# Kernel tuning notes

Measured on AMD Instinct MI355X. Metric: run time of the kernel, lower is better.

## Reference

```python
import jax, jax.numpy as jnp
import numpy as np

B, T, D, H, O = 64, 512, 256, 512, 256


def setup_inputs() -> dict:
    key = jax.random.key(0)
    ks = jax.random.split(key, 9)
    s = 0.05  # weight scale to keep activations in a sane range
    return {
        "x": jax.random.normal(ks[0], (B, T, D), jnp.float32),
        "h0": jax.random.normal(ks[1], (B, H), jnp.float32) * s,
        "c0": jax.random.normal(ks[2], (B, H), jnp.float32) * s,
        "W_x": jax.random.normal(ks[3], (D, 4 * H), jnp.float32) * s,
        "U_h": jax.random.normal(ks[4], (H, 4 * H), jnp.float32) * s,
        "b_ih": jax.random.normal(ks[5], (4 * H,), jnp.float32) * s,
        "b_hh": jax.random.normal(ks[6], (4 * H,), jnp.float32) * s,
        "W_y": jax.random.normal(ks[7], (H, O), jnp.float32) * s,
        "b_y": jax.random.normal(ks[8], (O,), jnp.float32) * s,
    }


def _lstm(x, h0, c0, W_x, U_h, b_ih, b_hh, W_y, b_y):
    Hd = h0.shape[-1]
    # hoist input projection out of the sequential loop: [B,T,4H]
    x_proj = jnp.einsum("btd,dg->btg", x, W_x) + b_ih + b_hh

    def step(carry, xp_t):
        h, c = carry
        gates = xp_t + h @ U_h  # [B,4H]
        i, f, j, o = jnp.split(gates, 4, axis=-1)
        i = jax.nn.sigmoid(i)
        f = jax.nn.sigmoid(f)
        j = jnp.tanh(j)
        o = jax.nn.sigmoid(o)
        c = f * c + i * j
        h = o * jnp.tanh(c)
        return (h, c), h

    (h_T, c_T), hs = jax.lax.scan(step, (h0, c0), jnp.swapaxes(x_proj, 0, 1))
    hs = jnp.swapaxes(hs, 0, 1)  # [B,T,H]
    y_hat = jnp.einsum("bth,ho->bto", hs, W_y) + b_y
    return y_hat, h_T, c_T


def reference(x, h0, c0, W_x, U_h, b_ih, b_hh, W_y, b_y):
    return _lstm(x, h0, c0, W_x, U_h, b_ih, b_hh, W_y, b_y)
```

## Files before the change

kernel.cpp:

```cpp
#include <hip/hip_runtime.h>

typedef short short8 __attribute__((ext_vector_type(8)));
typedef float f32x4 __attribute__((ext_vector_type(4)));

#define AS1 __attribute__((address_space(1)))
#define AS3 __attribute__((address_space(3)))

static constexpr size_t XP_OFF = 0;
static constexpr size_t HS_OFF = 134217728;
static constexpr size_t U_OFF  = 167772160;
static constexpr size_t WX_OFF = 169869312;
static constexpr size_t WY_OFF = 170917888;
static constexpr size_t BI_OFF = 171180032;
static constexpr size_t HB_OFF = 171188224;
static constexpr size_t FL_OFF = 171319296;
static constexpr size_t TB_OFF = 171323392;
static constexpr size_t PR_OFF = 171324416;
static constexpr size_t RS_OFF = 171328512;

static __device__ __forceinline__ unsigned short f2bf(float f) {
  unsigned u = __float_as_uint(f);
  unsigned r = (u + 0x7fffu + ((u >> 16) & 1u)) >> 16;
  return (unsigned short)r;
}
static __device__ __forceinline__ float bf2f(unsigned short s) {
  return __uint_as_float(((unsigned)s) << 16);
}
static __device__ __forceinline__ float sigf(float x) { return 1.0f / (1.0f + __expf(-x)); }
static __device__ __forceinline__ float tanhf_(float x) { return 1.0f - 2.0f / (1.0f + __expf(2.0f * x)); }

static __device__ __forceinline__ void gld_lds16(const void* g, void* l) {
  __builtin_amdgcn_global_load_lds((const AS1 unsigned int*)g, (AS3 unsigned int*)l, 16, 0, 0);
}
template<int SLOW>
static __device__ __forceinline__ void gld_lds16_c(const void* g, void* l) {
  if constexpr (SLOW)
    __builtin_amdgcn_global_load_lds((const AS1 unsigned int*)g, (AS3 unsigned int*)l, 16, 0, 17);
  else
    __builtin_amdgcn_global_load_lds((const AS1 unsigned int*)g, (AS3 unsigned int*)l, 16, 0, 1);
}
template<int SLOW>
static __device__ __forceinline__ unsigned ldflag(const unsigned* p) {
  unsigned r;
  if constexpr (SLOW)
    r = __hip_atomic_load(p, __ATOMIC_RELAXED, __HIP_MEMORY_SCOPE_AGENT);
  else
    asm volatile("global_load_dword %0, %1, off sc0\n\ts_waitcnt vmcnt(0)"
                 : "=v"(r) : "v"(p) : "memory");
  return r;
}
template<int SLOW>
static __device__ __forceinline__ void stflag(unsigned* p, unsigned v) {
  if constexpr (SLOW)
    __hip_atomic_store(p, v, __ATOMIC_RELAXED, __HIP_MEMORY_SCOPE_AGENT);
  else
    asm volatile("global_store_dword %0, %1, off sc0" :: "v"(p), "v"(v) : "memory");
}
template<int SLOW>
static __device__ __forceinline__ void sth32(void* p, unsigned v) {
  if constexpr (SLOW)
    __hip_atomic_store((unsigned*)p, v, __ATOMIC_RELAXED, __HIP_MEMORY_SCOPE_AGENT);
  else
    asm volatile("global_store_dword %0, %1, off sc0" :: "v"(p), "v"(v) : "memory");
}

#define DO16(M) M(0) M(1) M(2) M(3) M(4) M(5) M(6) M(7) M(8) M(9) M(10) M(11) \
  M(12) M(13) M(14) M(15)

static __device__ __forceinline__ unsigned orig_col(unsigned p) {
  return ((p & 127u) >> 5) * 512u + (p >> 7) * 32u + (p & 31u);
}

__global__ void prep_kernel(const float* __restrict__ Wx, const float* __restrict__ Uh,
                            const float* __restrict__ bih, const float* __restrict__ bhh,
                            const float* __restrict__ Wy, const float* __restrict__ h0,
                            char* __restrict__ ws) {
  unsigned idx0 = blockIdx.x * blockDim.x + threadIdx.x;
  unsigned stride = gridDim.x * blockDim.x;
  unsigned short* Up = (unsigned short*)(ws + U_OFF);
  for (unsigned i = idx0; i < 1048576u; i += stride) {
    unsigned k = i & 511u, p = i >> 9;
    Up[i] = f2bf(Uh[k * 2048u + orig_col(p)]);
  }
  unsigned short* Wxp = (unsigned short*)(ws + WX_OFF);
  for (unsigned i = idx0; i < 524288u; i += stride) {
    unsigned k = i & 255u, p = i >> 8;
    Wxp[i] = f2bf(Wx[k * 2048u + orig_col(p)]);
  }
  unsigned short* Wyp = (unsigned short*)(ws + WY_OFF);
  for (unsigned i = idx0; i < 131072u; i += stride) {
    unsigned k = i & 511u, n = i >> 9;
    Wyp[i] = f2bf(Wy[k * 256u + n]);
  }
  float* bp = (float*)(ws + BI_OFF);
  for (unsigned p = idx0; p < 2048u; p += stride) {
    unsigned c = orig_col(p);
    bp[p] = bih[c] + bhh[c];
  }
  unsigned short* hb = (unsigned short*)(ws + HB_OFF);
  for (unsigned i = idx0; i < 32768u; i += stride) hb[i] = f2bf(h0[i]);
  for (unsigned i = idx0; i < 3328u; i += stride)
    ((unsigned*)(ws + FL_OFF))[i] = 0u;
}

__launch_bounds__(256, 1)
__global__ void xproj_kernel(const float* __restrict__ x, char* __restrict__ ws) {
  extern __shared__ char smem[];
  char* a_lds = smem;
  char* b_lds = smem + 65536;
  const int tid = threadIdx.x, lane = tid & 63, wid = tid >> 6;
  const int wm = wid >> 1, wn = wid & 1;
  const int r0 = blockIdx.x * 128, p0 = blockIdx.y * 128;
  const unsigned short* WxT = (const unsigned short*)(ws + WX_OFF);

#pragma unroll
  for (int i = 0; i < 16; ++i) {
    int base = i * 4096 + wid * 1024;
    int byte = base + lane * 16;
    int row = byte >> 9;
    int kb = (byte >> 4) & 31;
    gld_lds16(WxT + (size_t)(p0 + row) * 256 + (size_t)((kb ^ (row & 15)) * 8), b_lds + base);
  }
  {
    int row = tid >> 1, half = tid & 1;
    const float* xr = x + (size_t)(r0 + row) * 256 + half * 128;
    char* ar = a_lds + row * 512;
#pragma unroll
    for (int i = 0; i < 16; ++i) {
      float4 f0 = *(const float4*)(xr + i * 8);
      float4 f1 = *(const float4*)(xr + i * 8 + 4);
      short8 v;
      v[0] = (short)f2bf(f0.x); v[1] = (short)f2bf(f0.y); v[2] = (short)f2bf(f0.z); v[3] = (short)f2bf(f0.w);
      v[4] = (short)f2bf(f1.x); v[5] = (short)f2bf(f1.y); v[6] = (short)f2bf(f1.z); v[7] = (short)f2bf(f1.w);
      int kb = half * 16 + i;
      *(short8*)(ar + ((kb ^ (row & 15)) * 16)) = v;
    }
  }
  __syncthreads();

  typedef float f32x16 __attribute__((ext_vector_type(16)));
  f32x16 acc[2][2] = {};
#pragma unroll
  for (int kk = 0; kk < 16; ++kk) {
    int kbW = kk * 2 + (lane >> 5);
    short8 a[2], b[2];
#pragma unroll
    for (int mt = 0; mt < 2; ++mt) {
      int row = wm * 64 + mt * 32 + (lane & 31);
      a[mt] = *(const short8*)(a_lds + row * 512 + ((kbW ^ (row & 15)) * 16));
    }
#pragma unroll
    for (int nt = 0; nt < 2; ++nt) {
      int n = wn * 64 + nt * 32 + (lane & 31);
      b[nt] = *(const short8*)(b_lds + n * 512 + ((kbW ^ (n & 15)) * 16));
    }
#pragma unroll
    for (int mt = 0; mt < 2; ++mt)
#pragma unroll
      for (int nt = 0; nt < 2; ++nt)
        acc[mt][nt] = __builtin_amdgcn_mfma_f32_32x32x16_bf16(a[mt], b[nt], acc[mt][nt], 0, 0, 0);
  }

  const float* bias = (const float*)(ws + BI_OFF);
  unsigned short* xp = (unsigned short*)(ws + XP_OFF);
#pragma unroll
  for (int nt = 0; nt < 2; ++nt) {
    int p = p0 + wn * 64 + nt * 32 + (lane & 31);
    float bv = bias[p];
    int g = p >> 7, q = p & 127;
#pragma unroll
    for (int mt = 0; mt < 2; ++mt) {
#pragma unroll
      for (int rg = 0; rg < 16; ++rg) {
        int r = r0 + wm * 64 + mt * 32 + (rg & 3) + 8 * (rg >> 2) + 4 * (lane >> 5);
        int b = r >> 9, t = r & 511;
        xp[((size_t)(t * 16 + g) * 64 + b) * 128 + q] = f2bf(acc[mt][nt][rg] + bv);
      }
    }
  }
}

template<int SLOW>
static __device__ __forceinline__ void run_loop(char* smem, const float* c0, char* ws,
                                                float* out, int tid, int ring, int g) {
  char* h_lds = smem;
  float* gates = (float*)(smem + 16384);
  const int lane = tid & 63, wid = tid >> 6;
  const int bq16 = ring * 16;
  char* hbuf = ws + HB_OFF;
  const unsigned short* xp = (const unsigned short*)(ws + XP_OFF);
  unsigned short* hs = (unsigned short*)(ws + HS_OFF);
  unsigned* flags = (unsigned*)(ws + FL_OFF);
  unsigned* myflag = flags + (size_t)(ring * 16 + g) * 16;
  unsigned* pollp = flags + (size_t)(ring * 16 + (lane & 15)) * 16;

  short8 bU[32];
  {
    const unsigned short* Up = (const unsigned short*)(ws + U_OFF);
    const unsigned short* pu0 = Up + (size_t)(g * 128 + wid * 32 + (lane & 15)) * 512 + (lane >> 4) * 8;
    const unsigned short* pu1 = pu0 + 16 * 512;
#define LDU0(k) asm volatile("global_load_dwordx4 %0, %1, off offset:%c2" \
                             : "=v"(bU[k]) : "v"(pu0), "i"((k) * 64) : "memory");
#define LDU1(k) asm volatile("global_load_dwordx4 %0, %1, off offset:%c2" \
                             : "=v"(bU[16 + (k)]) : "v"(pu1), "i"((k) * 64) : "memory");
    DO16(LDU0)
    DO16(LDU1)
#undef LDU0
#undef LDU1
    asm volatile("s_waitcnt vmcnt(0)" ::: "memory");
    __builtin_amdgcn_sched_barrier(0);
  }
  const int bl = tid >> 4, jlp = (tid & 15) * 2;
  float2 cp = *(const float2*)(c0 + (size_t)(bq16 + bl) * 512 + g * 32 + jlp);
  float cc0 = cp.x, cc1 = cp.y;

  for (int t = 0; t < 512; ++t) {
    const unsigned short* xpt = xp + ((size_t)(t * 16 + g) * 64 + (bq16 + bl)) * 128;
    ushort2 xi2 = *(const ushort2*)(xpt + jlp);
    ushort2 xf2 = *(const ushort2*)(xpt + 32 + jlp);
    ushort2 xj2 = *(const ushort2*)(xpt + 64 + jlp);
    ushort2 xo2 = *(const ushort2*)(xpt + 96 + jlp);

    if (wid == 0) {
      unsigned tgt = (unsigned)t;
      while (__any(ldflag<SLOW>(pollp) < tgt)) {}
    }
    __syncthreads();

    const char* hb = hbuf + (t & 1) * 65536;
#pragma unroll
    for (int i = 0; i < 4; ++i) {
      int r = wid * 4 + i;
      gld_lds16_c<SLOW>(hb + (size_t)(bq16 + r) * 1024 + ((lane ^ r) * 16), h_lds + r * 1024);
    }
    __syncthreads();

    f32x4 ac[2][2] = {};
#pragma unroll
    for (int ks = 0; ks < 16; ++ks) {
      int row = lane & 15;
      int gi = (ks * 4 + (lane >> 4)) ^ row;
      short8 a = *(const short8*)(h_lds + row * 1024 + gi * 16);
      ac[0][ks & 1] = __builtin_amdgcn_mfma_f32_16x16x32_bf16(a, bU[ks], ac[0][ks & 1], 0, 0, 0);
      ac[1][ks & 1] = __builtin_amdgcn_mfma_f32_16x16x32_bf16(a, bU[16 + ks], ac[1][ks & 1], 0, 0, 0);
    }
#pragma unroll
    for (int nt = 0; nt < 2; ++nt) {
      f32x4 acc = ac[nt][0] + ac[nt][1];
      int pl = wid * 32 + nt * 16 + (lane & 15);
      int rb = (lane >> 4) * 4;
#pragma unroll
      for (int rg = 0; rg < 4; ++rg)
        gates[(rb + rg) * 132 + pl] = acc[rg];
    }
    __syncthreads();

    const float* gr = gates + bl * 132;
    float2 gi2 = *(const float2*)(gr + jlp);
    float2 gf2 = *(const float2*)(gr + 32 + jlp);
    float2 gj2 = *(const float2*)(gr + 64 + jlp);
    float2 go2 = *(const float2*)(gr + 96 + jlp);
    float i0 = sigf(gi2.x + bf2f(xi2.x)), i1 = sigf(gi2.y + bf2f(xi2.y));
    float f0 = sigf(gf2.x + bf2f(xf2.x)), f1 = sigf(gf2.y + bf2f(xf2.y));
    float j0v = tanhf_(gj2.x + bf2f(xj2.x)), j1v = tanhf_(gj2.y + bf2f(xj2.y));
    float o0 = sigf(go2.x + bf2f(xo2.x)), o1 = sigf(go2.y + bf2f(xo2.y));
    cc0 = f0 * cc0 + i0 * j0v;
    cc1 = f1 * cc1 + i1 * j1v;
    float h0v = o0 * tanhf_(cc0);
    float h1v = o1 * tanhf_(cc1);
    unsigned hv = (unsigned)f2bf(h0v) | ((unsigned)f2bf(h1v) << 16);

    if (t < 511)
      sth32<SLOW>(hbuf + ((t + 1) & 1) * 65536 +
                  ((size_t)(bq16 + bl) * 512 + g * 32 + jlp) * 2, hv);
    *(unsigned*)(hs + ((size_t)(bq16 + bl) * 512 + t) * 512 + g * 32 + jlp) = hv;
    if (t == 511) {
      *(float2*)(out + 8388608u + (size_t)(bq16 + bl) * 512 + g * 32 + jlp) = make_float2(h0v, h1v);
      *(float2*)(out + 8421376u + (size_t)(bq16 + bl) * 512 + g * 32 + jlp) = make_float2(cc0, cc1);
    }
    asm volatile("s_waitcnt vmcnt(0)" ::: "memory");
    __syncthreads();
    if (tid == 0) stflag<SLOW>(myflag, (unsigned)(t + 1));
  }
}

__launch_bounds__(256, 1)
__global__ void lstm_rec_kernel(const float* __restrict__ c0, char* __restrict__ ws,
                                float* __restrict__ out) {
  extern __shared__ char smem[];
  unsigned* ldsT = (unsigned*)(smem + 16384 + 8448);
  unsigned* ldsF = (unsigned*)(smem + 16384 + 8448 + 1024);
  const int tid = threadIdx.x, lane = tid & 63, wid = tid >> 6;
  const int bid = blockIdx.x;

  unsigned* tbl = (unsigned*)(ws + TB_OFF);
  unsigned xcc;
  asm volatile("s_getreg_b32 %0, hwreg(HW_REG_XCC_ID)" : "=s"(xcc));
  if (tid == 0)
    __hip_atomic_store(tbl + bid, (xcc & 15u) + 1u, __ATOMIC_RELAXED, __HIP_MEMORY_SCOPE_AGENT);
  if (wid == 0) {
    for (;;) {
      unsigned v0 = __hip_atomic_load(tbl + lane, __ATOMIC_RELAXED, __HIP_MEMORY_SCOPE_AGENT);
      unsigned v1 = __hip_atomic_load(tbl + 64 + lane, __ATOMIC_RELAXED, __HIP_MEMORY_SCOPE_AGENT);
      unsigned v2 = __hip_atomic_load(tbl + 128 + lane, __ATOMIC_RELAXED, __HIP_MEMORY_SCOPE_AGENT);
      unsigned v3 = __hip_atomic_load(tbl + 192 + lane, __ATOMIC_RELAXED, __HIP_MEMORY_SCOPE_AGENT);
      ldsT[lane] = v0; ldsT[64 + lane] = v1; ldsT[128 + lane] = v2; ldsT[192 + lane] = v3;
      if (__all((v0 != 0u) && (v1 != 0u) && (v2 != 0u) && (v3 != 0u))) break;
    }
  }
  __syncthreads();

  int ringXcd[4] = {0, 0, 0, 0};
  int nr = 0;
  for (int x = 1; x <= 16; ++x) {
    int cnt = 0;
    for (int b = 0; b < 256; ++b) cnt += (ldsT[b] == (unsigned)x) ? 1 : 0;
    if (cnt >= 16 && nr < 4) ringXcd[nr++] = x;
  }
  bool slowForce = (nr < 4);
  int ring = 0, g = 0;
  bool sel = false;
  if (slowForce) {
    sel = (bid < 64);
    ring = bid >> 4;
    g = bid & 15;
  } else {
    unsigned myx = ldsT[bid];
    int r = -1;
    for (int i = 0; i < 4; ++i)
      if (ringXcd[i] == (int)myx) r = i;
    if (r >= 0) {
      int rank = 0;
      for (int b = 0; b < bid; ++b) rank += (ldsT[b] == myx) ? 1 : 0;
      if (rank < 16) { sel = true; ring = r; g = rank; }
    }
  }
  if (!sel) return;

  bool fast = false;
  if (!slowForce) {
    unsigned* probe = (unsigned*)(ws + PR_OFF);
    if (tid == 0) stflag<0>(probe + (size_t)(ring * 16 + g) * 16, 1u);
    asm volatile("s_waitcnt vmcnt(0)" ::: "memory");
    if (wid == 0) {
      int ok = 0;
      for (int it = 0; it < 4096; ++it) {
        unsigned v = ldflag<0>(probe + (size_t)(ring * 16 + (lane & 15)) * 16);
        if (__all(v != 0u)) { ok = 1; break; }
      }
      if (lane == 0) ldsF[0] = (unsigned)ok;
    }
    __syncthreads();
    unsigned ok = ldsF[0];
    unsigned* res = (unsigned*)(ws + RS_OFF);
    if (tid == 0) stflag<1>(res + (size_t)(ring * 16 + g) * 16, ok ? 2u : 1u);
    if (wid == 0) {
      unsigned v;
      do {
        v = ldflag<1>(res + (size_t)(ring * 16 + (lane & 15)) * 16);
      } while (__any(v == 0u));
      if (lane == 0) ldsF[1] = __all(v == 2u) ? 1u : 0u;
    }
    __syncthreads();
    fast = (ldsF[1] != 0u);
  }

  if (fast) run_loop<0>(smem, c0, (char*)ws, out, tid, ring, g);
  else      run_loop<1>(smem, c0, (char*)ws, out, tid, ring, g);
}

__launch_bounds__(256, 1)
__global__ void ygemm_kernel(const char* __restrict__ ws, const float* __restrict__ by,
                             float* __restrict__ out) {
  extern __shared__ char smem[];
  char* a_lds = smem;
  char* b_lds = smem + 32768;
  const int tid = threadIdx.x, lane = tid & 63, wid = tid >> 6;
  const int wm = wid >> 1, wn = wid & 1;
  const int r0 = blockIdx.x * 128, n0 = blockIdx.y * 128;
  const unsigned short* hs = (const unsigned short*)(ws + HS_OFF);
  const unsigned short* WyT = (const unsigned short*)(ws + WY_OFF);

  typedef float f32x16 __attribute__((ext_vector_type(16)));
  f32x16 acc[2][2] = {};
  for (int k0 = 0; k0 < 512; k0 += 128) {
#pragma unroll
    for (int i = 0; i < 8; ++i) {
      int base = i * 4096 + wid * 1024;
      int byte = base + lane * 16;
      int row = byte >> 8;
      int kb = (byte >> 4) & 15;
      gld_lds16(hs + (size_t)(r0 + row) * 512 + k0 + ((kb ^ (row & 15)) * 8), a_lds + base);
      gld_lds16(WyT + (size_t)(n0 + row) * 512 + k0 + ((kb ^ (row & 15)) * 8), b_lds + base);
    }
    __syncthreads();
#pragma unroll
    for (int kk = 0; kk < 8; ++kk) {
      int kbW = kk * 2 + (lane >> 5);
      short8 a[2], b[2];
#pragma unroll
      for (int mt = 0; mt < 2; ++mt) {
        int row = wm * 64 + mt * 32 + (lane & 31);
        a[mt] = *(const short8*)(a_lds + row * 256 + ((kbW ^ (row & 15)) * 16));
        int n = wn * 64 + mt * 32 + (lane & 31);
        b[mt] = *(const short8*)(b_lds + n * 256 + ((kbW ^ (n & 15)) * 16));
      }
#pragma unroll
      for (int mt = 0; mt < 2; ++mt)
#pragma unroll
        for (int nt = 0; nt < 2; ++nt)
          acc[mt][nt] = __builtin_amdgcn_mfma_f32_32x32x16_bf16(a[mt], b[nt], acc[mt][nt], 0, 0, 0);
    }
    __syncthreads();
  }
#pragma unroll
  for (int nt = 0; nt < 2; ++nt) {
    int o = n0 + wn * 64 + nt * 32 + (lane & 31);
    float bv = by[o];
#pragma unroll
    for (int mt = 0; mt < 2; ++mt)
#pragma unroll
      for (int rg = 0; rg < 16; ++rg) {
        int r = r0 + wm * 64 + mt * 32 + (rg & 3) + 8 * (rg >> 2) + 4 * (lane >> 5);
        out[(size_t)r * 256 + o] = acc[mt][nt][rg] + bv;
      }
  }
}

extern "C" void kernel_launch(void* const* d_in, const int* in_sizes, int n_in,
                              void* d_out, int out_size, void* d_ws, size_t ws_size,
                              hipStream_t stream) {
  (void)in_sizes; (void)n_in; (void)out_size; (void)ws_size;
  const float* x   = (const float*)d_in[0];
  const float* h0  = (const float*)d_in[1];
  const float* c0  = (const float*)d_in[2];
  const float* Wx  = (const float*)d_in[3];
  const float* Uh  = (const float*)d_in[4];
  const float* bih = (const float*)d_in[5];
  const float* bhh = (const float*)d_in[6];
  const float* Wy  = (const float*)d_in[7];
  const float* by  = (const float*)d_in[8];
  char* ws = (char*)d_ws;
  float* out = (float*)d_out;

  prep_kernel<<<1024, 256, 0, stream>>>(Wx, Uh, bih, bhh, Wy, h0, ws);
  xproj_kernel<<<dim3(256, 16), 256, 131072, stream>>>(x, ws);
  lstm_rec_kernel<<<256, 256, 16384 + 8448 + 1024 + 64, stream>>>(c0, ws, out);
  ygemm_kernel<<<dim3(256, 2), 256, 65536, stream>>>(ws, by, out);
}
```

Measured before the change: 1.746 ms.

## Use per-wave flags and stream h directly from global into MFMA

Replaces the per-block flag and two block barriers with per-wave progress flags, so each wave publishes its own step completion. Consumers poll all producer wave flags with a ballot mask and load each k-slice of h straight from global memory into registers once its producer chunk is ready. This lets MFMAs start on early chunks while later producers are still finishing, instead of waiting on LDS staging and block syncs. The cost is more flag traffic, four times as many flag slots, and finer-grained polling on the critical path.

```diff
diff --git a/kernel.cpp b/kernel.cpp
--- a/kernel.cpp
+++ b/kernel.cpp
@@ -14,9 +14,9 @@
 static constexpr size_t BI_OFF = 171180032;
 static constexpr size_t HB_OFF = 171188224;
 static constexpr size_t FL_OFF = 171319296;
-static constexpr size_t TB_OFF = 171323392;
-static constexpr size_t PR_OFF = 171324416;
-static constexpr size_t RS_OFF = 171328512;
+static constexpr size_t TB_OFF = 171335680;
+static constexpr size_t PR_OFF = 171336704;
+static constexpr size_t RS_OFF = 171340800;
 
 static __device__ __forceinline__ unsigned short f2bf(float f) {
   unsigned u = __float_as_uint(f);
@@ -33,17 +33,11 @@
   __builtin_amdgcn_global_load_lds((const AS1 unsigned int*)g, (AS3 unsigned int*)l, 16, 0, 0);
 }
 template<int SLOW>
-static __device__ __forceinline__ void gld_lds16_c(const void* g, void* l) {
-  if constexpr (SLOW)
-    __builtin_amdgcn_global_load_lds((const AS1 unsigned int*)g, (AS3 unsigned int*)l, 16, 0, 17);
-  else
-    __builtin_amdgcn_global_load_lds((const AS1 unsigned int*)g, (AS3 unsigned int*)l, 16, 0, 1);
-}
-template<int SLOW>
 static __device__ __forceinline__ unsigned ldflag(const unsigned* p) {
   unsigned r;
   if constexpr (SLOW)
-    r = __hip_atomic_load(p, __ATOMIC_RELAXED, __HIP_MEMORY_SCOPE_AGENT);
+    asm volatile("global_load_dword %0, %1, off sc0 sc1\n\ts_waitcnt vmcnt(0)"
+                 : "=v"(r) : "v"(p) : "memory");
   else
     asm volatile("global_load_dword %0, %1, off sc0\n\ts_waitcnt vmcnt(0)"
                  : "=v"(r) : "v"(p) : "memory");
@@ -99,7 +93,7 @@
   }
   unsigned short* hb = (unsigned short*)(ws + HB_OFF);
   for (unsigned i = idx0; i < 32768u; i += stride) hb[i] = f2bf(h0[i]);
-  for (unsigned i = idx0; i < 3328u; i += stride)
+  for (unsigned i = idx0; i < 6400u; i += stride)
     ((unsigned*)(ws + FL_OFF))[i] = 0u;
 }
 
@@ -183,16 +177,15 @@
 template<int SLOW>
 static __device__ __forceinline__ void run_loop(char* smem, const float* c0, char* ws,
                                                 float* out, int tid, int ring, int g) {
-  char* h_lds = smem;
-  float* gates = (float*)(smem + 16384);
+  float* gates = (float*)smem;
   const int lane = tid & 63, wid = tid >> 6;
   const int bq16 = ring * 16;
   char* hbuf = ws + HB_OFF;
   const unsigned short* xp = (const unsigned short*)(ws + XP_OFF);
   unsigned short* hs = (unsigned short*)(ws + HS_OFF);
   unsigned* flags = (unsigned*)(ws + FL_OFF);
-  unsigned* myflag = flags + (size_t)(ring * 16 + g) * 16;
-  unsigned* pollp = flags + (size_t)(ring * 16 + (lane & 15)) * 16;
+  unsigned* myflag = flags + ((size_t)(ring * 16 + g) * 4 + wid) * 16;
+  const unsigned* pollw = flags + ((size_t)(ring * 16 + (lane >> 2)) * 4 + (lane & 3)) * 16;
 
   short8 bU[32];
   {
@@ -213,6 +206,7 @@
   const int bl = tid >> 4, jlp = (tid & 15) * 2;
   float2 cp = *(const float2*)(c0 + (size_t)(bq16 + bl) * 512 + g * 32 + jlp);
   float cc0 = cp.x, cc1 = cp.y;
+  const char* paB = hbuf + (size_t)(bq16 + (lane & 15)) * 1024 + (lane >> 4) * 16;
 
   for (int t = 0; t < 512; ++t) {
     const unsigned short* xpt = xp + ((size_t)(t * 16 + g) * 64 + (bq16 + bl)) * 128;
@@ -221,37 +215,74 @@
     ushort2 xj2 = *(const ushort2*)(xpt + 64 + jlp);
     ushort2 xo2 = *(const ushort2*)(xpt + 96 + jlp);
 
-    if (wid == 0) {
-      unsigned tgt = (unsigned)t;
-      while (__any(ldflag<SLOW>(pollp) < tgt)) {}
-    }
-    __syncthreads();
-
-    const char* hb = hbuf + (t & 1) * 65536;
-#pragma unroll
-    for (int i = 0; i < 4; ++i) {
-      int r = wid * 4 + i;
-      gld_lds16_c<SLOW>(hb + (size_t)(bq16 + r) * 1024 + ((lane ^ r) * 16), h_lds + r * 1024);
-    }
-    __syncthreads();
-
+    const char* pa = paB + (t & 1) * 65536;
+    const unsigned tgt = (unsigned)t;
+    unsigned long long bm;
+    {
+      unsigned v0 = ldflag<SLOW>(pollw);
+      bm = __ballot(v0 >= tgt);
+    }
     f32x4 ac[2][2] = {};
-#pragma unroll
-    for (int ks = 0; ks < 16; ++ks) {
-      int row = lane & 15;
-      int gi = (ks * 4 + (lane >> 4)) ^ row;
-      short8 a = *(const short8*)(h_lds + row * 1024 + gi * 16);
-      ac[0][ks & 1] = __builtin_amdgcn_mfma_f32_16x16x32_bf16(a, bU[ks], ac[0][ks & 1], 0, 0, 0);
-      ac[1][ks & 1] = __builtin_amdgcn_mfma_f32_16x16x32_bf16(a, bU[16 + ks], ac[1][ks & 1], 0, 0, 0);
-    }
+    short8 F0, F1, F2;
+#define WAITK(ks) while (((bm >> (4 * (ks))) & 15ull) != 15ull) {                \
+      unsigned v_ = ldflag<SLOW>(pollw);                                         \
+      bm = __ballot(v_ >= tgt);                                                  \
+    }
+#define LOADF(R, ks) do {                                                        \
+      if constexpr (SLOW)                                                        \
+        asm volatile("global_load_dwordx4 %0, %1, off offset:%c2 sc0 sc1"        \
+                     : "=v"(R) : "v"(pa), "i"((ks) * 64) : "memory");            \
+      else                                                                       \
+        asm volatile("global_load_dwordx4 %0, %1, off offset:%c2 sc0"            \
+                     : "=v"(R) : "v"(pa), "i"((ks) * 64) : "memory");            \
+    } while (0)
+#define MM2(CUR, ks)                                                             \
+    ac[0][(ks) & 1] = __builtin_amdgcn_mfma_f32_16x16x32_bf16(CUR, bU[(ks)], ac[0][(ks) & 1], 0, 0, 0); \
+    ac[1][(ks) & 1] = __builtin_amdgcn_mfma_f32_16x16x32_bf16(CUR, bU[16 + (ks)], ac[1][(ks) & 1], 0, 0, 0);
+#define STEPK(ks, CUR, NX)                                                       \
+    WAITK((ks) + 2)                                                              \
+    LOADF(NX, (ks) + 2);                                                         \
+    asm volatile("s_waitcnt vmcnt(2)" ::: "memory");                             \
+    __builtin_amdgcn_sched_barrier(0);                                           \
+    MM2(CUR, ks)
+
+    WAITK(0)
+    LOADF(F0, 0);
+    WAITK(1)
+    LOADF(F1, 1);
+    STEPK(0, F0, F2)
+    STEPK(1, F1, F0)
+    STEPK(2, F2, F1)
+    STEPK(3, F0, F2)
+    STEPK(4, F1, F0)
+    STEPK(5, F2, F1)
+    STEPK(6, F0, F2)
+    STEPK(7, F1, F0)
+    STEPK(8, F2, F1)
+    STEPK(9, F0, F2)
+    STEPK(10, F1, F0)
+    STEPK(11, F2, F1)
+    STEPK(12, F0, F2)
+    STEPK(13, F1, F0)
+    asm volatile("s_waitcnt vmcnt(1)" ::: "memory");
+    __builtin_amdgcn_sched_barrier(0);
+    MM2(F2, 14)
+    asm volatile("s_waitcnt vmcnt(0)" ::: "memory");
+    __builtin_amdgcn_sched_barrier(0);
+    MM2(F0, 15)
+#undef STEPK
+#undef MM2
+#undef LOADF
+#undef WAITK
+
 #pragma unroll
     for (int nt = 0; nt < 2; ++nt) {
-      f32x4 acc = ac[nt][0] + ac[nt][1];
+      f32x4 facc = ac[nt][0] + ac[nt][1];
       int pl = wid * 32 + nt * 16 + (lane & 15);
       int rb = (lane >> 4) * 4;
 #pragma unroll
       for (int rg = 0; rg < 4; ++rg)
-        gates[(rb + rg) * 132 + pl] = acc[rg];
+        gates[(rb + rg) * 132 + pl] = facc[rg];
     }
     __syncthreads();
 
@@ -273,14 +304,13 @@
     if (t < 511)
       sth32<SLOW>(hbuf + ((t + 1) & 1) * 65536 +
                   ((size_t)(bq16 + bl) * 512 + g * 32 + jlp) * 2, hv);
+    asm volatile("s_waitcnt vmcnt(0)" ::: "memory");
+    if ((lane & 63) == 0) stflag<SLOW>(myflag, (unsigned)(t + 1));
     *(unsigned*)(hs + ((size_t)(bq16 + bl) * 512 + t) * 512 + g * 32 + jlp) = hv;
     if (t == 511) {
       *(float2*)(out + 8388608u + (size_t)(bq16 + bl) * 512 + g * 32 + jlp) = make_float2(h0v, h1v);
       *(float2*)(out + 8421376u + (size_t)(bq16 + bl) * 512 + g * 32 + jlp) = make_float2(cc0, cc1);
     }
-    asm volatile("s_waitcnt vmcnt(0)" ::: "memory");
-    __syncthreads();
-    if (tid == 0) stflag<SLOW>(myflag, (unsigned)(t + 1));
   }
 }
 
@@ -288,8 +318,8 @@
 __global__ void lstm_rec_kernel(const float* __restrict__ c0, char* __restrict__ ws,
                                 float* __restrict__ out) {
   extern __shared__ char smem[];
-  unsigned* ldsT = (unsigned*)(smem + 16384 + 8448);
-  unsigned* ldsF = (unsigned*)(smem + 16384 + 8448 + 1024);
+  unsigned* ldsT = (unsigned*)smem;
+  unsigned* ldsF = (unsigned*)(smem + 1024);
   const int tid = threadIdx.x, lane = tid & 63, wid = tid >> 6;
   const int bid = blockIdx.x;
 
@@ -357,13 +387,15 @@
     if (wid == 0) {
       unsigned v;
       do {
-        v = ldflag<1>(res + (size_t)(ring * 16 + (lane & 15)) * 16);
+        v = __hip_atomic_load((unsigned*)(ws + RS_OFF) + (size_t)(ring * 16 + (lane & 15)) * 16,
+                              __ATOMIC_RELAXED, __HIP_MEMORY_SCOPE_AGENT);
       } while (__any(v == 0u));
       if (lane == 0) ldsF[1] = __all(v == 2u) ? 1u : 0u;
     }
     __syncthreads();
     fast = (ldsF[1] != 0u);
   }
+  __syncthreads();
 
   if (fast) run_loop<0>(smem, c0, (char*)ws, out, tid, ring, g);
   else      run_loop<1>(smem, c0, (char*)ws, out, tid, ring, g);
@@ -445,6 +477,6 @@
 
   prep_kernel<<<1024, 256, 0, stream>>>(Wx, Uh, bih, bhh, Wy, h0, ws);
   xproj_kernel<<<dim3(256, 16), 256, 131072, stream>>>(x, ws);
-  lstm_rec_kernel<<<256, 256, 16384 + 8448 + 1024 + 64, stream>>>(c0, ws, out);
+  lstm_rec_kernel<<<256, 256, 8448, stream>>>(c0, ws, out);
   ygemm_kernel<<<dim3(256, 2), 256, 65536, stream>>>(ws, by, out);
 }
```

New measurement: 2.567 ms. 47.0% more time.

## Remove per-step block barriers in LSTM recurrence via per-wave flags and in-register gates

Applied to the files above, without the earlier changes.

Reorders the gate columns so that each wave's MFMA output already holds the i,f,j,o values for its own hidden units. Gates are then combined with lane shuffles in registers instead of through an LDS gates buffer guarded by two __syncthreads. Each wave publishes its own progress flag and every wave polls all 64 producer flags, and the h tile in LDS is double-buffered. Together these remove most block-wide barriers from the sequential 512-step loop. The cost is more flag traffic (64 flags polled per wave, larger flag region to clear) and more shuffle work.

```diff
diff --git a/kernel.cpp b/kernel.cpp
--- a/kernel.cpp
+++ b/kernel.cpp
@@ -14,9 +14,9 @@
 static constexpr size_t BI_OFF = 171180032;
 static constexpr size_t HB_OFF = 171188224;
 static constexpr size_t FL_OFF = 171319296;
-static constexpr size_t TB_OFF = 171323392;
-static constexpr size_t PR_OFF = 171324416;
-static constexpr size_t RS_OFF = 171328512;
+static constexpr size_t TB_OFF = 171581440;
+static constexpr size_t PR_OFF = 171582464;
+static constexpr size_t RS_OFF = 171586560;
 
 static __device__ __forceinline__ unsigned short f2bf(float f) {
   unsigned u = __float_as_uint(f);
@@ -43,7 +43,8 @@
 static __device__ __forceinline__ unsigned ldflag(const unsigned* p) {
   unsigned r;
   if constexpr (SLOW)
-    r = __hip_atomic_load(p, __ATOMIC_RELAXED, __HIP_MEMORY_SCOPE_AGENT);
+    asm volatile("global_load_dword %0, %1, off sc0 sc1\n\ts_waitcnt vmcnt(0)"
+                 : "=v"(r) : "v"(p) : "memory");
   else
     asm volatile("global_load_dword %0, %1, off sc0\n\ts_waitcnt vmcnt(0)"
                  : "=v"(r) : "v"(p) : "memory");
@@ -57,18 +58,22 @@
     asm volatile("global_store_dword %0, %1, off sc0" :: "v"(p), "v"(v) : "memory");
 }
 template<int SLOW>
-static __device__ __forceinline__ void sth32(void* p, unsigned v) {
+static __device__ __forceinline__ void sth64(void* p, unsigned long long v) {
   if constexpr (SLOW)
-    __hip_atomic_store((unsigned*)p, v, __ATOMIC_RELAXED, __HIP_MEMORY_SCOPE_AGENT);
+    __hip_atomic_store((unsigned long long*)p, v, __ATOMIC_RELAXED, __HIP_MEMORY_SCOPE_AGENT);
   else
-    asm volatile("global_store_dword %0, %1, off sc0" :: "v"(p), "v"(v) : "memory");
+    asm volatile("global_store_dwordx2 %0, %1, off sc0" :: "v"(p), "v"(v) : "memory");
 }
 
 #define DO16(M) M(0) M(1) M(2) M(3) M(4) M(5) M(6) M(7) M(8) M(9) M(10) M(11) \
   M(12) M(13) M(14) M(15)
 
 static __device__ __forceinline__ unsigned orig_col(unsigned p) {
-  return ((p & 127u) >> 5) * 512u + (p >> 7) * 32u + (p & 31u);
+  unsigned pw = p & 127u, g = p >> 7;
+  unsigned wid = pw >> 5, n = (pw >> 4) & 1u, c = pw & 15u;
+  unsigned gate = n * 2u + (c >> 3);
+  unsigned jl = wid * 8u + (c & 7u);
+  return gate * 512u + g * 32u + jl;
 }
 
 __global__ void prep_kernel(const float* __restrict__ Wx, const float* __restrict__ Uh,
@@ -99,7 +104,7 @@
   }
   unsigned short* hb = (unsigned short*)(ws + HB_OFF);
   for (unsigned i = idx0; i < 32768u; i += stride) hb[i] = f2bf(h0[i]);
-  for (unsigned i = idx0; i < 3328u; i += stride)
+  for (unsigned i = idx0; i < 67840u; i += stride)
     ((unsigned*)(ws + FL_OFF))[i] = 0u;
 }
 
@@ -167,14 +172,18 @@
   for (int nt = 0; nt < 2; ++nt) {
     int p = p0 + wn * 64 + nt * 32 + (lane & 31);
     float bv = bias[p];
-    int g = p >> 7, q = p & 127;
+    int g = p >> 7, pw = p & 127;
+    int widp = pw >> 5, np = (pw >> 4) & 1, cq = pw & 15;
+    int gate = np * 2 + (cq >> 3);
+    int jl = widp * 8 + (cq & 7);
+    int qx = jl * 4 + gate;
 #pragma unroll
     for (int mt = 0; mt < 2; ++mt) {
 #pragma unroll
       for (int rg = 0; rg < 16; ++rg) {
         int r = r0 + wm * 64 + mt * 32 + (rg & 3) + 8 * (rg >> 2) + 4 * (lane >> 5);
         int b = r >> 9, t = r & 511;
-        xp[((size_t)(t * 16 + g) * 64 + b) * 128 + q] = f2bf(acc[mt][nt][rg] + bv);
+        xp[((size_t)(t * 16 + g) * 64 + b) * 128 + qx] = f2bf(acc[mt][nt][rg] + bv);
       }
     }
   }
@@ -183,16 +192,15 @@
 template<int SLOW>
 static __device__ __forceinline__ void run_loop(char* smem, const float* c0, char* ws,
                                                 float* out, int tid, int ring, int g) {
-  char* h_lds = smem;
-  float* gates = (float*)(smem + 16384);
+  char* h_lds2 = smem;
   const int lane = tid & 63, wid = tid >> 6;
   const int bq16 = ring * 16;
   char* hbuf = ws + HB_OFF;
   const unsigned short* xp = (const unsigned short*)(ws + XP_OFF);
   unsigned short* hs = (unsigned short*)(ws + HS_OFF);
   unsigned* flags = (unsigned*)(ws + FL_OFF);
-  unsigned* myflag = flags + (size_t)(ring * 16 + g) * 16;
-  unsigned* pollp = flags + (size_t)(ring * 16 + (lane & 15)) * 16;
+  unsigned* pubp = flags + ((size_t)(ring * 16 + (lane & 15)) * 64 + (g * 4 + wid)) * 16;
+  const unsigned* pollp = flags + ((size_t)(ring * 16 + g) * 64 + lane) * 16;
 
   short8 bU[32];
   {
@@ -210,28 +218,35 @@
     asm volatile("s_waitcnt vmcnt(0)" ::: "memory");
     __builtin_amdgcn_sched_barrier(0);
   }
-  const int bl = tid >> 4, jlp = (tid & 15) * 2;
-  float2 cp = *(const float2*)(c0 + (size_t)(bq16 + bl) * 512 + g * 32 + jlp);
-  float cc0 = cp.x, cc1 = cp.y;
+
+  const int c = lane & 15, rg = lane >> 4;
+  const bool active = (c < 8);
+  const int jl = wid * 8 + (c & 7);
+  const int q = (c >> 2) & 1;
+  const bool odd = (c & 1), hi = ((c >> 1) & 1);
+  float cc[4];
+#pragma unroll
+  for (int r = 0; r < 4; ++r)
+    cc[r] = c0[(size_t)(bq16 + 4 * rg + r) * 512 + g * 32 + jl];
 
   for (int t = 0; t < 512; ++t) {
-    const unsigned short* xpt = xp + ((size_t)(t * 16 + g) * 64 + (bq16 + bl)) * 128;
-    ushort2 xi2 = *(const ushort2*)(xpt + jlp);
-    ushort2 xf2 = *(const ushort2*)(xpt + 32 + jlp);
-    ushort2 xj2 = *(const ushort2*)(xpt + 64 + jlp);
-    ushort2 xo2 = *(const ushort2*)(xpt + 96 + jlp);
-
-    if (wid == 0) {
+    const unsigned short* xpt = xp + ((size_t)(t * 16 + g) * 64 + (bq16 + 4 * rg)) * 128 + jl * 4;
+    ushort4 xg0 = *(const ushort4*)(xpt);
+    ushort4 xg1 = *(const ushort4*)(xpt + 128);
+    ushort4 xg2 = *(const ushort4*)(xpt + 256);
+    ushort4 xg3 = *(const ushort4*)(xpt + 384);
+
+    {
       unsigned tgt = (unsigned)t;
-      while (__any(ldflag<SLOW>(pollp) < tgt)) {}
-    }
-    __syncthreads();
-
+      unsigned v = ldflag<SLOW>(pollp);
+      while (!__all(v >= tgt)) v = ldflag<SLOW>(pollp);
+    }
+    char* hl = h_lds2 + (t & 1) * 16384;
     const char* hb = hbuf + (t & 1) * 65536;
 #pragma unroll
     for (int i = 0; i < 4; ++i) {
       int r = wid * 4 + i;
-      gld_lds16_c<SLOW>(hb + (size_t)(bq16 + r) * 1024 + ((lane ^ r) * 16), h_lds + r * 1024);
+      gld_lds16_c<SLOW>(hb + (size_t)(bq16 + r) * 1024 + ((lane ^ r) * 16), hl + r * 1024);
     }
     __syncthreads();
 
@@ -239,48 +254,66 @@
 #pragma unroll
     for (int ks = 0; ks < 16; ++ks) {
       int row = lane & 15;
-      int gi = (ks * 4 + (lane >> 4)) ^ row;
-      short8 a = *(const short8*)(h_lds + row * 1024 + gi * 16);
+      int gi = (ks * 4 + rg) ^ row;
+      short8 a = *(const short8*)(hl + row * 1024 + gi * 16);
       ac[0][ks & 1] = __builtin_amdgcn_mfma_f32_16x16x32_bf16(a, bU[ks], ac[0][ks & 1], 0, 0, 0);
       ac[1][ks & 1] = __builtin_amdgcn_mfma_f32_16x16x32_bf16(a, bU[16 + ks], ac[1][ks & 1], 0, 0, 0);
     }
-#pragma unroll
-    for (int nt = 0; nt < 2; ++nt) {
-      f32x4 acc = ac[nt][0] + ac[nt][1];
-      int pl = wid * 32 + nt * 16 + (lane & 15);
-      int rb = (lane >> 4) * 4;
-#pragma unroll
-      for (int rg = 0; rg < 4; ++rg)
-        gates[(rb + rg) * 132 + pl] = acc[rg];
-    }
-    __syncthreads();
-
-    const float* gr = gates + bl * 132;
-    float2 gi2 = *(const float2*)(gr + jlp);
-    float2 gf2 = *(const float2*)(gr + 32 + jlp);
-    float2 gj2 = *(const float2*)(gr + 64 + jlp);
-    float2 go2 = *(const float2*)(gr + 96 + jlp);
-    float i0 = sigf(gi2.x + bf2f(xi2.x)), i1 = sigf(gi2.y + bf2f(xi2.y));
-    float f0 = sigf(gf2.x + bf2f(xf2.x)), f1 = sigf(gf2.y + bf2f(xf2.y));
-    float j0v = tanhf_(gj2.x + bf2f(xj2.x)), j1v = tanhf_(gj2.y + bf2f(xj2.y));
-    float o0 = sigf(go2.x + bf2f(xo2.x)), o1 = sigf(go2.y + bf2f(xo2.y));
-    cc0 = f0 * cc0 + i0 * j0v;
-    cc1 = f1 * cc1 + i1 * j1v;
-    float h0v = o0 * tanhf_(cc0);
-    float h1v = o1 * tanhf_(cc1);
-    unsigned hv = (unsigned)f2bf(h0v) | ((unsigned)f2bf(h1v) << 16);
-
-    if (t < 511)
-      sth32<SLOW>(hbuf + ((t + 1) & 1) * 65536 +
-                  ((size_t)(bq16 + bl) * 512 + g * 32 + jlp) * 2, hv);
-    *(unsigned*)(hs + ((size_t)(bq16 + bl) * 512 + t) * 512 + g * 32 + jlp) = hv;
-    if (t == 511) {
-      *(float2*)(out + 8388608u + (size_t)(bq16 + bl) * 512 + g * 32 + jlp) = make_float2(h0v, h1v);
-      *(float2*)(out + 8421376u + (size_t)(bq16 + bl) * 512 + g * 32 + jlp) = make_float2(cc0, cc1);
+    f32x4 f0v = ac[0][0] + ac[0][1];
+    f32x4 f1v = ac[1][0] + ac[1][1];
+    f32x4 o0v, o1v;
+#pragma unroll
+    for (int r = 0; r < 4; ++r) {
+      o0v[r] = __shfl_xor(f0v[r], 8);
+      o1v[r] = __shfl_xor(f1v[r], 8);
+    }
+    float v0, v1, v2, v3;
+    {
+      float iv, fv, jv, ov, cn;
+      iv = sigf(f0v[0] + bf2f(xg0.x)); fv = sigf(o0v[0] + bf2f(xg0.y));
+      jv = tanhf_(f1v[0] + bf2f(xg0.z)); ov = sigf(o1v[0] + bf2f(xg0.w));
+      cn = fv * cc[0] + iv * jv; cc[0] = cn; v0 = ov * tanhf_(cn);
+      iv = sigf(f0v[1] + bf2f(xg1.x)); fv = sigf(o0v[1] + bf2f(xg1.y));
+      jv = tanhf_(f1v[1] + bf2f(xg1.z)); ov = sigf(o1v[1] + bf2f(xg1.w));
+      cn = fv * cc[1] + iv * jv; cc[1] = cn; v1 = ov * tanhf_(cn);
+      iv = sigf(f0v[2] + bf2f(xg2.x)); fv = sigf(o0v[2] + bf2f(xg2.y));
+      jv = tanhf_(f1v[2] + bf2f(xg2.z)); ov = sigf(o1v[2] + bf2f(xg2.w));
+      cn = fv * cc[2] + iv * jv; cc[2] = cn; v2 = ov * tanhf_(cn);
+      iv = sigf(f0v[3] + bf2f(xg3.x)); fv = sigf(o0v[3] + bf2f(xg3.y));
+      jv = tanhf_(f1v[3] + bf2f(xg3.z)); ov = sigf(o1v[3] + bf2f(xg3.w));
+      cn = fv * cc[3] + iv * jv; cc[3] = cn; v3 = ov * tanhf_(cn);
+    }
+    {
+      float sA0 = odd ? v0 : v1, sA1 = odd ? v2 : v3;
+      float rA0 = __shfl_xor(sA0, 1), rA1 = __shfl_xor(sA1, 1);
+      v0 = odd ? rA0 : v0;  v1 = odd ? v1 : rA0;
+      v2 = odd ? rA1 : v2;  v3 = odd ? v3 : rA1;
+      float sB0 = hi ? v0 : v2, sB1 = hi ? v1 : v3;
+      float rB0 = __shfl_xor(sB0, 2), rB1 = __shfl_xor(sB1, 2);
+      v0 = hi ? rB0 : v0;  v1 = hi ? rB1 : v1;
+      v2 = hi ? v2 : rB0;  v3 = hi ? v3 : rB1;
+    }
+    const int bT = bq16 + 4 * rg + (c & 3);
+    const int jT = g * 32 + wid * 8 + 4 * q;
+    unsigned long long hpk;
+    {
+      union { unsigned short u[4]; unsigned long long ll; } pk;
+      pk.u[0] = f2bf(v0); pk.u[1] = f2bf(v1); pk.u[2] = f2bf(v2); pk.u[3] = f2bf(v3);
+      hpk = pk.ll;
+    }
+    if (active) {
+      sth64<SLOW>(hbuf + ((t + 1) & 1) * 65536 + (size_t)bT * 1024 + (size_t)jT * 2, hpk);
+      if (t == 511) {
+        *(float4*)(out + 8388608u + (size_t)bT * 512 + jT) = make_float4(v0, v1, v2, v3);
+#pragma unroll
+        for (int r = 0; r < 4; ++r)
+          out[8421376u + (size_t)(bq16 + 4 * rg + r) * 512 + g * 32 + jl] = cc[r];
+      }
     }
     asm volatile("s_waitcnt vmcnt(0)" ::: "memory");
-    __syncthreads();
-    if (tid == 0) stflag<SLOW>(myflag, (unsigned)(t + 1));
+    if ((lane & 63) < 16) stflag<SLOW>(pubp, (unsigned)(t + 1));
+    if (active)
+      *(unsigned long long*)(hs + ((size_t)bT * 512 + t) * 512 + jT) = hpk;
   }
 }
 
@@ -288,8 +321,8 @@
 __global__ void lstm_rec_kernel(const float* __restrict__ c0, char* __restrict__ ws,
                                 float* __restrict__ out) {
   extern __shared__ char smem[];
-  unsigned* ldsT = (unsigned*)(smem + 16384 + 8448);
-  unsigned* ldsF = (unsigned*)(smem + 16384 + 8448 + 1024);
+  unsigned* ldsT = (unsigned*)smem;
+  unsigned* ldsF = (unsigned*)(smem + 1024);
   const int tid = threadIdx.x, lane = tid & 63, wid = tid >> 6;
   const int bid = blockIdx.x;
 
@@ -357,13 +390,15 @@
     if (wid == 0) {
       unsigned v;
       do {
-        v = ldflag<1>(res + (size_t)(ring * 16 + (lane & 15)) * 16);
+        v = __hip_atomic_load((unsigned*)(ws + RS_OFF) + (size_t)(ring * 16 + (lane & 15)) * 16,
+                              __ATOMIC_RELAXED, __HIP_MEMORY_SCOPE_AGENT);
       } while (__any(v == 0u));
       if (lane == 0) ldsF[1] = __all(v == 2u) ? 1u : 0u;
     }
     __syncthreads();
     fast = (ldsF[1] != 0u);
   }
+  __syncthreads();
 
   if (fast) run_loop<0>(smem, c0, (char*)ws, out, tid, ring, g);
   else      run_loop<1>(smem, c0, (char*)ws, out, tid, ring, g);
@@ -445,6 +480,6 @@
 
   prep_kernel<<<1024, 256, 0, stream>>>(Wx, Uh, bih, bhh, Wy, h0, ws);
   xproj_kernel<<<dim3(256, 16), 256, 131072, stream>>>(x, ws);
-  lstm_rec_kernel<<<256, 256, 16384 + 8448 + 1024 + 64, stream>>>(c0, ws, out);
+  lstm_rec_kernel<<<256, 256, 32768, stream>>>(c0, ws, out);
   ygemm_kernel<<<dim3(256, 2), 256, 65536, stream>>>(ws, by, out);
 }
```

Measured after the change: 2.618 ms. 1.5x slower.
